# Kernel optimization log

Measured on AMD Instinct MI355X. Metric: run time of the kernel, lower is better.

The kernel has to match this reference:

```python
import jax, jax.numpy as jnp
import numpy as np
import math

L, H, NH, DH, E, FF, A, I = 3, 1024, 8, 128, 768, 4096, 100, 50
B, S = 4, 1024
EPS = 1e-5


def _ln(x, g, b):
    m = jnp.mean(x, -1, keepdims=True)
    v = jnp.var(x, -1, keepdims=True)
    return (x - m) * jax.lax.rsqrt(v + EPS) * g + b


def _pos_encoding(seq, d):
    pos = jnp.arange(seq, dtype=jnp.float32)[:, None]
    div = jnp.exp(jnp.arange(0, d, 2, dtype=jnp.float32) * (-math.log(10000.0) / d))
    ang = pos * div  # [S, d/2]
    return jnp.stack([jnp.sin(ang), jnp.cos(ang)], axis=-1).reshape(seq, d)


def setup_inputs() -> dict:
    key = jax.random.key(0)
    ks = jax.random.split(key, 40)
    w = lambda k, s: jax.random.normal(k, s, jnp.float32) * 0.02
    z = lambda s: jnp.zeros(s, jnp.float32)
    d = {}
    d['frame_embeddings'] = jax.random.normal(ks[0], (B, S, E), jnp.float32)
    d['W_in'] = w(ks[1], (H, E)); d['b_in'] = z((H,))
    # _init_weights sets ALL 'weight' params (incl. LayerNorm) to normal(std=0.02)
    d['ln_in_g'] = w(ks[2], (H,)); d['ln_in_b'] = z((H,))
    d['qkv_w'] = w(ks[3], (L, 3 * H, H)); d['qkv_b'] = z((L, 3 * H))
    d['out_w'] = w(ks[4], (L, H, H)); d['out_b'] = z((L, H))
    d['ff1_w'] = w(ks[5], (L, FF, H)); d['ff1_b'] = z((L, FF))
    d['ff2_w'] = w(ks[6], (L, H, FF)); d['ff2_b'] = z((L, H))
    d['n1_g'] = w(ks[7], (L, H)); d['n1_b'] = z((L, H))
    d['n2_g'] = w(ks[8], (L, H)); d['n2_b'] = z((L, H))
    d['ln_out_g'] = w(ks[9], (H,)); d['ln_out_b'] = z((H,))
    d['a1_w'] = w(ks[10], (H, H)); d['a1_b'] = z((H,))
    d['a2_w'] = w(ks[11], (A, H)); d['a2_b'] = z((A,))
    d['i1_w'] = w(ks[12], (H, H)); d['i1_b'] = z((H,))
    d['i2_w'] = w(ks[13], (I, H)); d['i2_b'] = z((I,))
    d['c1_w'] = w(ks[14], (H // 2, H)); d['c1_b'] = z((H // 2,))
    d['c2_w'] = w(ks[15], (1, H // 2)); d['c2_b'] = z((1,))
    d['p_w'] = w(ks[16], (1, H)); d['p_b'] = z((1,))
    d['smoothing_factor'] = jnp.float32(0.7)
    return d


def _encoder_layer(x, qkv_w, qkv_b, out_w, out_b, ff1_w, ff1_b, ff2_w, ff2_b, n1_g, n1_b, n2_g, n2_b):
    # PyTorch post-norm TransformerEncoderLayer (eval: no dropout)
    b, s, _ = x.shape
    qkv = x @ qkv_w.T + qkv_b  # [B,S,3H]
    q, k, v = jnp.split(qkv, 3, axis=-1)
    q = q.reshape(b, s, NH, DH)
    k = k.reshape(b, s, NH, DH)
    v = v.reshape(b, s, NH, DH)
    scores = jnp.einsum('bqhd,bkhd->bhqk', q, k) / math.sqrt(DH)
    attn = jax.nn.softmax(scores, axis=-1)
    ctx = jnp.einsum('bhqk,bkhd->bqhd', attn, v).reshape(b, s, H)
    x = _ln(x + (ctx @ out_w.T + out_b), n1_g, n1_b)
    ff = jax.nn.gelu(x @ ff1_w.T + ff1_b, approximate=False) @ ff2_w.T + ff2_b
    return _ln(x + ff, n2_g, n2_b)


def reference(frame_embeddings, W_in, b_in, ln_in_g, ln_in_b, qkv_w, qkv_b, out_w, out_b,
              ff1_w, ff1_b, ff2_w, ff2_b, n1_g, n1_b, n2_g, n2_b, ln_out_g, ln_out_b,
              a1_w, a1_b, a2_w, a2_b, i1_w, i1_b, i2_w, i2_b, c1_w, c1_b, c2_w, c2_b,
              p_w, p_b, smoothing_factor):
    b, s, _ = frame_embeddings.shape
    h = frame_embeddings @ W_in.T + b_in
    h = h + _pos_encoding(s, H)[None]
    h = _ln(h, ln_in_g, ln_in_b)
    for l in range(L):
        h = _encoder_layer(h, qkv_w[l], qkv_b[l], out_w[l], out_b[l], ff1_w[l], ff1_b[l],
                           ff2_w[l], ff2_b[l], n1_g[l], n1_b[l], n2_g[l], n2_b[l])
    ctx = _ln(h, ln_out_g, ln_out_b)
    action = jax.nn.gelu(ctx @ a1_w.T + a1_b, approximate=False) @ a2_w.T + a2_b  # [B,S,A]
    instr = jax.nn.gelu(ctx @ i1_w.T + i1_b, approximate=False) @ i2_w.T + i2_b  # [B,S,I]
    conf = jax.nn.sigmoid(jax.nn.gelu(ctx @ c1_w.T + c1_b, approximate=False) @ c2_w.T + c2_b)
    # EMA smoothing over time as a single scan (replaces the per-step Python loop)
    sf = jnp.clip(smoothing_factor, 0.0, 1.0)
    both = jnp.concatenate([action, instr], axis=-1)  # [B,S,A+I]
    def step(carry, xt):
        sm = sf * xt + (1.0 - sf) * carry
        return sm, sm
    _, ys = jax.lax.scan(step, both[:, 0], jnp.swapaxes(both[:, 1:], 0, 1))
    smoothed = jnp.concatenate([both[:, :1], jnp.swapaxes(ys, 0, 1)], axis=1)
    action = smoothed[..., :A]
    instr = smoothed[..., A:]
    pool = jax.nn.softmax(ctx @ p_w.T + p_b, axis=1)  # [B,S,1]
    global_ctx = jnp.einsum('bsi,bsh->bih', pool, ctx)[:, 0]  # [B,H]
    return action, instr, conf, pool[..., 0], global_ctx
```

## Files before the change

kernel.cpp:

```cpp
#include <hip/hip_runtime.h>

typedef __attribute__((ext_vector_type(8))) short frag8;
typedef __attribute__((ext_vector_type(4))) float facc4;

#define MFMA16(a,b,c) __builtin_amdgcn_mfma_f32_16x16x32_bf16((a),(b),(c),0,0,0)

__device__ __forceinline__ unsigned short f2bf(float f){
  unsigned int u = __builtin_bit_cast(unsigned int, f);
  u += 0x7FFFu + ((u >> 16) & 1u);
  return (unsigned short)(u >> 16);
}
__device__ __forceinline__ float bf2f(unsigned short h){
  unsigned int u = ((unsigned int)h) << 16;
  return __builtin_bit_cast(float, u);
}
__device__ __forceinline__ float gelu_f(float x){
  return 0.5f * x * (1.0f + erff(x * 0.70710678118654752440f));
}
__device__ __forceinline__ void gload16(const void* g, void* l){
  __builtin_amdgcn_global_load_lds(
      (const __attribute__((address_space(1))) void*)g,
      (__attribute__((address_space(3))) void*)l, 16, 0, 0);
}

struct CvtSeg { const float* src; unsigned short* dst; long total; long blk_start; int rows_src; int K; };
struct CvtArgs { CvtSeg seg[12]; int nseg; };

__global__ void convert_all(CvtArgs a){
  long blk = blockIdx.x;
  int si = 0;
  for (int i = 1; i < a.nseg; i++) if (blk >= a.seg[i].blk_start) si = i;
  CvtSeg s = a.seg[si];
  long i = ((blk - s.blk_start) * 256 + threadIdx.x) * 4L;
  if (i >= s.total) return;
  long row = i / s.K;
  ushort4 o;
  if (row < s.rows_src){
    float4 v = *(const float4*)(s.src + i);
    o.x = f2bf(v.x); o.y = f2bf(v.y); o.z = f2bf(v.z); o.w = f2bf(v.w);
  } else { o.x = 0; o.y = 0; o.z = 0; o.w = 0; }
  *(ushort4*)(s.dst + i) = o;
}

__global__ void pe_kernel(float* __restrict__ pe){
  const int s = blockIdx.x;
  const int t = threadIdx.x;
  float4 o;
#pragma unroll
  for (int e = 0; e < 4; e++){
    int c = t * 4 + e;
    int i2 = c & ~1;
    float dv = expf(-0.0089944730195080f * (float)i2);
    float ang = (float)s * dv;
    ((float*)&o)[e] = (c & 1) ? cosf(ang) : sinf(ang);
  }
  *(float4*)(pe + (size_t)s * 1024 + t * 4) = o;
}

template<int EPI>
__global__ __launch_bounds__(256, 2)
void gemm_bt(const unsigned short* __restrict__ A,
             const unsigned short* __restrict__ W,
             const float* __restrict__ bias,
             void* __restrict__ Cout,
             int K, int ldC, int coloff, int nvalid)
{
  __shared__ unsigned short As[128 * 32];
  __shared__ unsigned short Bs[128 * 32];
  const int tid = threadIdx.x;
  const int w = tid >> 6, lane = tid & 63;
  const int lh = lane & 15, lq = lane >> 4;
  const int wr = w >> 1, wc = w & 1;
  const long row0 = (long)blockIdx.x * 128;
  const long col0 = (long)blockIdx.y * 128;

  facc4 acc[4][4];
  const facc4 vz = {0.f, 0.f, 0.f, 0.f};
#pragma unroll
  for (int r = 0; r < 4; r++)
#pragma unroll
    for (int c = 0; c < 4; c++) acc[r][c] = vz;

  const int arow = w * 16 + (lane >> 2);
  const int aseg = (lane & 3) * 8;
  const unsigned short* A0 = A + (row0 + arow) * (long)K + aseg;
  const unsigned short* A1 = A + (row0 + 64 + arow) * (long)K + aseg;
  const unsigned short* W0 = W + (col0 + arow) * (long)K + aseg;
  const unsigned short* W1 = W + (col0 + 64 + arow) * (long)K + aseg;
  char* lA0 = (char*)As + w * 1024;
  char* lA1 = (char*)As + 4096 + w * 1024;
  char* lB0 = (char*)Bs + w * 1024;
  char* lB1 = (char*)Bs + 4096 + w * 1024;

  for (int k0 = 0; k0 < K; k0 += 32){
    gload16(A0 + k0, lA0);
    gload16(A1 + k0, lA1);
    gload16(W0 + k0, lB0);
    gload16(W1 + k0, lB1);
    __syncthreads();
    frag8 af[4], bf[4];
#pragma unroll
    for (int r = 0; r < 4; r++) af[r] = *(const frag8*)&As[(wr * 64 + r * 16 + lh) * 32 + lq * 8];
#pragma unroll
    for (int c = 0; c < 4; c++) bf[c] = *(const frag8*)&Bs[(wc * 64 + c * 16 + lh) * 32 + lq * 8];
#pragma unroll
    for (int r = 0; r < 4; r++)
#pragma unroll
      for (int c = 0; c < 4; c++)
        acc[r][c] = MFMA16(af[r], bf[c], acc[r][c]);
    __syncthreads();
  }

#pragma unroll
  for (int c = 0; c < 4; c++){
    const int colt = wc * 64 + c * 16 + lh;
    const long gcol = col0 + colt;
    const bool ok = gcol < nvalid;
    const float bv = ok ? bias[gcol] : 0.f;
#pragma unroll
    for (int r = 0; r < 4; r++){
#pragma unroll
      for (int j = 0; j < 4; j++){
        if (!ok) continue;
        const long grow = row0 + wr * 64 + r * 16 + lq * 4 + j;
        float v = acc[r][c][j] + bv;
        if (EPI == 2) v = gelu_f(v);
        const long off = grow * (long)ldC + coloff + gcol;
        if (EPI == 0) ((float*)Cout)[off] = v;
        else          ((unsigned short*)Cout)[off] = f2bf(v);
      }
    }
  }
}

__global__ __launch_bounds__(256)
void ln_kernel(const float* __restrict__ a, const float* __restrict__ bsrc, int bmode,
               const float* __restrict__ g, const float* __restrict__ be,
               float* __restrict__ of32, unsigned short* __restrict__ obf)
{
  const int row = blockIdx.x;
  const int t = threadIdx.x;
  float4 x = ((const float4*)(a + (size_t)row * 1024))[t];
  if (bmode){
    const size_t brow = (bmode == 1) ? (size_t)row : (size_t)(row & 1023);
    float4 y = ((const float4*)(bsrc + brow * 1024))[t];
    x.x += y.x; x.y += y.y; x.z += y.z; x.w += y.w;
  }
  float s = x.x + x.y + x.z + x.w;
  float ss = x.x * x.x + x.y * x.y + x.z * x.z + x.w * x.w;
#pragma unroll
  for (int mk = 1; mk < 64; mk <<= 1){ s += __shfl_xor(s, mk); ss += __shfl_xor(ss, mk); }
  __shared__ float red[8];
  const int w = t >> 6, lane = t & 63;
  if (lane == 0){ red[w] = s; red[4 + w] = ss; }
  __syncthreads();
  s = red[0] + red[1] + red[2] + red[3];
  ss = red[4] + red[5] + red[6] + red[7];
  const float mean = s * (1.f / 1024.f);
  const float var = ss * (1.f / 1024.f) - mean * mean;
  const float rstd = rsqrtf(var + 1e-5f);
  float4 gg = ((const float4*)g)[t];
  float4 bb = ((const float4*)be)[t];
  float4 o;
  o.x = (x.x - mean) * rstd * gg.x + bb.x;
  o.y = (x.y - mean) * rstd * gg.y + bb.y;
  o.z = (x.z - mean) * rstd * gg.z + bb.z;
  o.w = (x.w - mean) * rstd * gg.w + bb.w;
  if (of32) ((float4*)(of32 + (size_t)row * 1024))[t] = o;
  if (obf){
    ushort4 hh;
    hh.x = f2bf(o.x); hh.y = f2bf(o.y); hh.z = f2bf(o.z); hh.w = f2bf(o.w);
    ((ushort4*)(obf + (size_t)row * 1024))[t] = hh;
  }
}

__global__ void transpose_v(const unsigned short* __restrict__ qkv, unsigned short* __restrict__ vt){
  __shared__ unsigned short t[32][33];
  const int s0 = blockIdx.x * 32;
  const int d0 = blockIdx.y * 32;
  const int bh = blockIdx.z;
  const int b = bh >> 3, h = bh & 7;
  const int tx = threadIdx.x, ty = threadIdx.y;
#pragma unroll
  for (int j = 0; j < 4; j++){
    int srow = ty + j * 8;
    t[srow][tx] = qkv[(size_t)(b * 1024 + s0 + srow) * 3072 + 2048 + h * 128 + d0 + tx];
  }
  __syncthreads();
#pragma unroll
  for (int j = 0; j < 4; j++){
    int drow = ty + j * 8;
    vt[((size_t)bh * 128 + d0 + drow) * 1024 + s0 + tx] = t[tx][drow];
  }
}

__global__ __launch_bounds__(256, 1)
void attn_kernel(const unsigned short* __restrict__ qkv,
                 const unsigned short* __restrict__ vt,
                 unsigned short* __restrict__ ctx)
{
  const int qt = blockIdx.x, h = blockIdx.y, b = blockIdx.z;
  const int tid = threadIdx.x;
  const int w = tid >> 6, lane = tid & 63;
  const int lh = lane & 15, lq = lane >> 4;
  __shared__ unsigned short P[4][32][136];

  const float scale = 0.08838834764831845f;
  const size_t qbase = (size_t)b * 1024 * 3072 + (size_t)h * 128;
  const int q0 = qt * 128 + w * 32;

  frag8 qf[2][4];
#pragma unroll
  for (int r = 0; r < 2; r++)
#pragma unroll
    for (int kk = 0; kk < 4; kk++)
      qf[r][kk] = *(const frag8*)(qkv + qbase + (size_t)(q0 + r * 16 + lh) * 3072 + kk * 32 + lq * 8);

  facc4 O[2][8];
  const facc4 vz = {0.f, 0.f, 0.f, 0.f};
#pragma unroll
  for (int r = 0; r < 2; r++)
#pragma unroll
    for (int c = 0; c < 8; c++) O[r][c] = vz;
  float m[2][4], l[2][4];
#pragma unroll
  for (int r = 0; r < 2; r++)
#pragma unroll
    for (int j = 0; j < 4; j++){ m[r][j] = -3.0e38f; l[r][j] = 0.f; }

  for (int kv0 = 0; kv0 < 1024; kv0 += 128){
    facc4 S[2][8];
#pragma unroll
    for (int r = 0; r < 2; r++)
#pragma unroll
      for (int c = 0; c < 8; c++) S[r][c] = vz;
#pragma unroll
    for (int c = 0; c < 8; c++){
      frag8 kf[4];
#pragma unroll
      for (int kk = 0; kk < 4; kk++)
        kf[kk] = *(const frag8*)(qkv + qbase + 1024 + (size_t)(kv0 + c * 16 + lh) * 3072 + kk * 32 + lq * 8);
#pragma unroll
      for (int kk = 0; kk < 4; kk++)
#pragma unroll
        for (int r = 0; r < 2; r++)
          S[r][c] = MFMA16(qf[r][kk], kf[kk], S[r][c]);
    }
    float tmax[2][4];
#pragma unroll
    for (int r = 0; r < 2; r++)
#pragma unroll
      for (int j = 0; j < 4; j++) tmax[r][j] = -3.0e38f;
#pragma unroll
    for (int r = 0; r < 2; r++)
#pragma unroll
      for (int c = 0; c < 8; c++)
#pragma unroll
        for (int j = 0; j < 4; j++){
          float v = S[r][c][j] * scale;
          S[r][c][j] = v;
          tmax[r][j] = fmaxf(tmax[r][j], v);
        }
#pragma unroll
    for (int mk = 1; mk < 16; mk <<= 1)
#pragma unroll
      for (int r = 0; r < 2; r++)
#pragma unroll
        for (int j = 0; j < 4; j++)
          tmax[r][j] = fmaxf(tmax[r][j], __shfl_xor(tmax[r][j], mk));
    float al[2][4], rs[2][4];
#pragma unroll
    for (int r = 0; r < 2; r++)
#pragma unroll
      for (int j = 0; j < 4; j++){
        float mn = fmaxf(m[r][j], tmax[r][j]);
        al[r][j] = __expf(m[r][j] - mn);
        m[r][j] = mn;
        rs[r][j] = 0.f;
      }
#pragma unroll
    for (int r = 0; r < 2; r++)
#pragma unroll
      for (int c = 0; c < 8; c++)
#pragma unroll
        for (int j = 0; j < 4; j++){
          float p = __expf(S[r][c][j] - m[r][j]);
          S[r][c][j] = p;
          rs[r][j] += p;
        }
#pragma unroll
    for (int mk = 1; mk < 16; mk <<= 1)
#pragma unroll
      for (int r = 0; r < 2; r++)
#pragma unroll
        for (int j = 0; j < 4; j++)
          rs[r][j] += __shfl_xor(rs[r][j], mk);
#pragma unroll
    for (int r = 0; r < 2; r++)
#pragma unroll
      for (int j = 0; j < 4; j++) l[r][j] = l[r][j] * al[r][j] + rs[r][j];
#pragma unroll
    for (int r = 0; r < 2; r++)
#pragma unroll
      for (int c = 0; c < 8; c++)
#pragma unroll
        for (int j = 0; j < 4; j++) O[r][c][j] *= al[r][j];
#pragma unroll
    for (int r = 0; r < 2; r++)
#pragma unroll
      for (int c = 0; c < 8; c++)
#pragma unroll
        for (int j = 0; j < 4; j++)
          P[w][r * 16 + lq * 4 + j][c * 16 + lh] = f2bf(S[r][c][j]);
    frag8 pf[2][4];
#pragma unroll
    for (int r = 0; r < 2; r++)
#pragma unroll
      for (int kk = 0; kk < 4; kk++)
        pf[r][kk] = *(const frag8*)&P[w][r * 16 + lh][kk * 32 + lq * 8];
#pragma unroll
    for (int c2 = 0; c2 < 8; c2++){
      frag8 vf[4];
#pragma unroll
      for (int kk = 0; kk < 4; kk++)
        vf[kk] = *(const frag8*)(vt + ((size_t)(b * 8 + h) * 128 + c2 * 16 + lh) * 1024 + kv0 + kk * 32 + lq * 8);
#pragma unroll
      for (int kk = 0; kk < 4; kk++)
#pragma unroll
        for (int r = 0; r < 2; r++)
          O[r][c2] = MFMA16(pf[r][kk], vf[kk], O[r][c2]);
    }
  }
#pragma unroll
  for (int r = 0; r < 2; r++)
#pragma unroll
    for (int c2 = 0; c2 < 8; c2++)
#pragma unroll
      for (int j = 0; j < 4; j++)
        P[w][r * 16 + lq * 4 + j][c2 * 16 + lh] = f2bf(O[r][c2][j] / l[r][j]);
  for (int rr = 0; rr < 32; rr++){
    const int token = b * 1024 + qt * 128 + w * 32 + rr;
    const unsigned int val = *(const unsigned int*)&P[w][rr][lane * 2];
    *(unsigned int*)(ctx + (size_t)token * 1024 + h * 128 + lane * 2) = val;
  }
}

__global__ void ema_kernel(const float* __restrict__ both, const float* __restrict__ sfp,
                           float* __restrict__ oact, float* __restrict__ oinst)
{
  const int idx = blockIdx.x * 256 + threadIdx.x;
  if (idx >= 4 * 1024 * 150) return;
  const int c = idx % 150;
  const int bs = idx / 150;
  const int s = bs & 1023;
  float sf = fminf(fmaxf(sfp[0], 0.f), 1.f);
  const float q = 1.f - sf;
  const float* p = both + (size_t)bs * 160 + c;
  float acc = 0.f, wgt = sf;
  const int klim = (s < 28) ? s : 28;
  for (int k = 0; k < klim; k++){ acc += wgt * p[-(long)k * 160]; wgt *= q; }
  if (s <= 28) acc += powf(q, (float)s) * p[-(long)s * 160];
  if (c < 100) oact[(size_t)bs * 100 + c] = acc;
  else         oinst[(size_t)bs * 50 + (c - 100)] = acc;
}

__global__ void head_c2(const unsigned short* __restrict__ x, const float* __restrict__ wv,
                        const float* __restrict__ bv, float* __restrict__ out)
{
  const int row = blockIdx.x * 4 + (threadIdx.x >> 6);
  const int lane = threadIdx.x & 63;
  float acc = 0.f;
#pragma unroll
  for (int i = 0; i < 8; i++){
    int cidx = i * 64 + lane;
    acc += bf2f(x[(size_t)row * 512 + cidx]) * wv[cidx];
  }
#pragma unroll
  for (int mk = 1; mk < 64; mk <<= 1) acc += __shfl_xor(acc, mk);
  if (lane == 0) out[row] = 1.f / (1.f + __expf(-(acc + bv[0])));
}

__global__ void head_p(const float* __restrict__ x, const float* __restrict__ wv,
                       const float* __restrict__ bv, float* __restrict__ out)
{
  const int row = blockIdx.x * 4 + (threadIdx.x >> 6);
  const int lane = threadIdx.x & 63;
  float acc = 0.f;
#pragma unroll
  for (int i = 0; i < 16; i++){
    int cidx = i * 64 + lane;
    acc += x[(size_t)row * 1024 + cidx] * wv[cidx];
  }
#pragma unroll
  for (int mk = 1; mk < 64; mk <<= 1) acc += __shfl_xor(acc, mk);
  if (lane == 0) out[row] = acc + bv[0];
}

__global__ void pool_softmax(const float* __restrict__ scores, float* __restrict__ poolws,
                             float* __restrict__ outpool)
{
  const int b = blockIdx.x, t = threadIdx.x;
  float4 v = ((const float4*)(scores + (size_t)b * 1024))[t];
  float mx = fmaxf(fmaxf(v.x, v.y), fmaxf(v.z, v.w));
#pragma unroll
  for (int mk = 1; mk < 64; mk <<= 1) mx = fmaxf(mx, __shfl_xor(mx, mk));
  __shared__ float red[8];
  const int w = t >> 6, lane = t & 63;
  if (lane == 0) red[w] = mx;
  __syncthreads();
  mx = fmaxf(fmaxf(red[0], red[1]), fmaxf(red[2], red[3]));
  float4 e;
  e.x = __expf(v.x - mx); e.y = __expf(v.y - mx); e.z = __expf(v.z - mx); e.w = __expf(v.w - mx);
  float sum = e.x + e.y + e.z + e.w;
#pragma unroll
  for (int mk = 1; mk < 64; mk <<= 1) sum += __shfl_xor(sum, mk);
  if (lane == 0) red[4 + w] = sum;
  __syncthreads();
  sum = red[4] + red[5] + red[6] + red[7];
  const float inv = 1.f / sum;
  e.x *= inv; e.y *= inv; e.z *= inv; e.w *= inv;
  ((float4*)(poolws + (size_t)b * 1024))[t] = e;
  ((float4*)(outpool + (size_t)b * 1024))[t] = e;
}

__global__ void globalctx_kernel(const float* __restrict__ pool, const float* __restrict__ ctxf,
                                 float* __restrict__ out)
{
  const int hh = blockIdx.x * 256 + threadIdx.x;
  const int b = blockIdx.y;
  const float* p = pool + (size_t)b * 1024;
  const float* c = ctxf + (size_t)b * 1024 * 1024 + hh;
  float acc = 0.f;
  for (int s = 0; s < 1024; s++) acc += p[s] * c[(size_t)s * 1024];
  out[(size_t)b * 1024 + hh] = acc;
}

extern "C" void kernel_launch(void* const* d_in, const int* in_sizes, int n_in,
                              void* d_out, int out_size, void* d_ws, size_t ws_size,
                              hipStream_t stream)
{
  if (n_in < 34) return;
  const float* emb     = (const float*)d_in[0];
  const float* W_in    = (const float*)d_in[1];
  const float* b_in    = (const float*)d_in[2];
  const float* ln_in_g = (const float*)d_in[3];
  const float* ln_in_b = (const float*)d_in[4];
  const float* qkv_w   = (const float*)d_in[5];
  const float* qkv_b   = (const float*)d_in[6];
  const float* out_w   = (const float*)d_in[7];
  const float* out_b   = (const float*)d_in[8];
  const float* ff1_w   = (const float*)d_in[9];
  const float* ff1_b   = (const float*)d_in[10];
  const float* ff2_w   = (const float*)d_in[11];
  const float* ff2_b   = (const float*)d_in[12];
  const float* n1_g    = (const float*)d_in[13];
  const float* n1_b    = (const float*)d_in[14];
  const float* n2_g    = (const float*)d_in[15];
  const float* n2_b    = (const float*)d_in[16];
  const float* ln_out_g= (const float*)d_in[17];
  const float* ln_out_b= (const float*)d_in[18];
  const float* a1_w    = (const float*)d_in[19];
  const float* a1_b    = (const float*)d_in[20];
  const float* a2_w    = (const float*)d_in[21];
  const float* a2_b    = (const float*)d_in[22];
  const float* i1_w    = (const float*)d_in[23];
  const float* i1_b    = (const float*)d_in[24];
  const float* i2_w    = (const float*)d_in[25];
  const float* i2_b    = (const float*)d_in[26];
  const float* c1_w    = (const float*)d_in[27];
  const float* c1_b    = (const float*)d_in[28];
  const float* c2_w    = (const float*)d_in[29];
  const float* c2_b    = (const float*)d_in[30];
  const float* p_w     = (const float*)d_in[31];
  const float* p_b     = (const float*)d_in[32];
  const float* sfp     = (const float*)d_in[33];

  char* ws = (char*)d_ws;
  size_t off = 0;
  auto alloc = [&](size_t bytes) -> void* {
    void* p = ws + off;
    off += (bytes + 255) & ~(size_t)255;
    return p;
  };
  unsigned short* emb_bf  = (unsigned short*)alloc((size_t)4096 * 768 * 2);
  unsigned short* Win_bf  = (unsigned short*)alloc((size_t)1024 * 768 * 2);
  unsigned short* qkvw_bf = (unsigned short*)alloc((size_t)3 * 3072 * 1024 * 2);
  unsigned short* outw_bf = (unsigned short*)alloc((size_t)3 * 1024 * 1024 * 2);
  unsigned short* ff1w_bf = (unsigned short*)alloc((size_t)3 * 4096 * 1024 * 2);
  unsigned short* ff2w_bf = (unsigned short*)alloc((size_t)3 * 1024 * 4096 * 2);
  unsigned short* a1w_bf  = (unsigned short*)alloc((size_t)1024 * 1024 * 2);
  unsigned short* a2w_bf  = (unsigned short*)alloc((size_t)128 * 1024 * 2);
  unsigned short* i1w_bf  = (unsigned short*)alloc((size_t)1024 * 1024 * 2);
  unsigned short* i2w_bf  = (unsigned short*)alloc((size_t)128 * 1024 * 2);
  unsigned short* c1w_bf  = (unsigned short*)alloc((size_t)512 * 1024 * 2);
  float* pe      = (float*)alloc((size_t)1024 * 1024 * 4);
  float* t0      = (float*)alloc((size_t)4096 * 1024 * 4);
  float* hres    = (float*)alloc((size_t)4096 * 1024 * 4);
  unsigned short* h_bf = (unsigned short*)alloc((size_t)4096 * 1024 * 2);
  unsigned short* buf1 = (unsigned short*)alloc((size_t)4096 * 4096 * 2);
  unsigned short* vtb  = (unsigned short*)alloc((size_t)4096 * 1024 * 2);
  unsigned short* ctxb = (unsigned short*)alloc((size_t)4096 * 1024 * 2);
  float* bothb  = (float*)alloc((size_t)4096 * 160 * 4);
  float* scores = (float*)alloc((size_t)4096 * 4);
  float* poolws = (float*)alloc((size_t)4096 * 4);
  if (off > ws_size) return;

  float* out_action = (float*)d_out;
  float* out_instr  = out_action + 4 * 1024 * 100;
  float* out_conf   = out_instr + 4 * 1024 * 50;
  float* out_pool   = out_conf + 4 * 1024;
  float* out_gctx   = out_pool + 4 * 1024;

  CvtArgs ca{};
  long blk = 0;
  auto addseg = [&](const float* src, unsigned short* dst, long rows_src, long rows_dst, long Kd){
    CvtSeg& sg = ca.seg[ca.nseg];
    sg.src = src; sg.dst = dst; sg.total = rows_dst * Kd;
    sg.rows_src = (int)rows_src; sg.K = (int)Kd; sg.blk_start = blk;
    blk += (sg.total + 1023) / 1024;
    ca.nseg++;
  };
  addseg(emb,   emb_bf,  4096, 4096, 768);
  addseg(W_in,  Win_bf,  1024, 1024, 768);
  addseg(qkv_w, qkvw_bf, 9216, 9216, 1024);
  addseg(out_w, outw_bf, 3072, 3072, 1024);
  addseg(ff1_w, ff1w_bf, 12288, 12288, 1024);
  addseg(ff2_w, ff2w_bf, 3072, 3072, 4096);
  addseg(a1_w,  a1w_bf,  1024, 1024, 1024);
  addseg(a2_w,  a2w_bf,  100,  128,  1024);
  addseg(i1_w,  i1w_bf,  1024, 1024, 1024);
  addseg(i2_w,  i2w_bf,  50,   128,  1024);
  addseg(c1_w,  c1w_bf,  512,  512,  1024);
  convert_all<<<dim3((unsigned)blk), dim3(256), 0, stream>>>(ca);

  pe_kernel<<<dim3(1024), dim3(256), 0, stream>>>(pe);

  gemm_bt<0><<<dim3(32, 8), dim3(256), 0, stream>>>(emb_bf, Win_bf, b_in, t0, 768, 1024, 0, 1024);
  ln_kernel<<<dim3(4096), dim3(256), 0, stream>>>(t0, pe, 2, ln_in_g, ln_in_b, hres, h_bf);

  for (int l = 0; l < 3; l++){
    gemm_bt<1><<<dim3(32, 24), dim3(256), 0, stream>>>(h_bf, qkvw_bf + (size_t)l * 3072 * 1024,
                                                       qkv_b + (size_t)l * 3072, buf1, 1024, 3072, 0, 3072);
    transpose_v<<<dim3(32, 4, 32), dim3(32, 8), 0, stream>>>(buf1, vtb);
    attn_kernel<<<dim3(8, 8, 4), dim3(256), 0, stream>>>(buf1, vtb, ctxb);
    gemm_bt<0><<<dim3(32, 8), dim3(256), 0, stream>>>(ctxb, outw_bf + (size_t)l * 1024 * 1024,
                                                      out_b + (size_t)l * 1024, t0, 1024, 1024, 0, 1024);
    ln_kernel<<<dim3(4096), dim3(256), 0, stream>>>(hres, t0, 1, n1_g + l * 1024, n1_b + l * 1024, hres, h_bf);
    gemm_bt<2><<<dim3(32, 32), dim3(256), 0, stream>>>(h_bf, ff1w_bf + (size_t)l * 4096 * 1024,
                                                       ff1_b + (size_t)l * 4096, buf1, 1024, 4096, 0, 4096);
    gemm_bt<0><<<dim3(32, 8), dim3(256), 0, stream>>>(buf1, ff2w_bf + (size_t)l * 1024 * 4096,
                                                      ff2_b + (size_t)l * 1024, t0, 4096, 1024, 0, 1024);
    ln_kernel<<<dim3(4096), dim3(256), 0, stream>>>(hres, t0, 1, n2_g + l * 1024, n2_b + l * 1024, hres, h_bf);
  }

  ln_kernel<<<dim3(4096), dim3(256), 0, stream>>>(hres, nullptr, 0, ln_out_g, ln_out_b, t0, ctxb);

  gemm_bt<2><<<dim3(32, 8), dim3(256), 0, stream>>>(ctxb, a1w_bf, a1_b, vtb, 1024, 1024, 0, 1024);
  gemm_bt<0><<<dim3(32, 1), dim3(256), 0, stream>>>(vtb, a2w_bf, a2_b, bothb, 1024, 160, 0, 100);
  gemm_bt<2><<<dim3(32, 8), dim3(256), 0, stream>>>(ctxb, i1w_bf, i1_b, vtb, 1024, 1024, 0, 1024);
  gemm_bt<0><<<dim3(32, 1), dim3(256), 0, stream>>>(vtb, i2w_bf, i2_b, bothb, 1024, 160, 100, 50);
  gemm_bt<2><<<dim3(32, 4), dim3(256), 0, stream>>>(ctxb, c1w_bf, c1_b, vtb, 1024, 512, 0, 512);
  head_c2<<<dim3(1024), dim3(256), 0, stream>>>(vtb, c2_w, c2_b, out_conf);
  head_p<<<dim3(1024), dim3(256), 0, stream>>>(t0, p_w, p_b, scores);
  pool_softmax<<<dim3(4), dim3(256), 0, stream>>>(scores, poolws, out_pool);
  globalctx_kernel<<<dim3(4, 4), dim3(256), 0, stream>>>(poolws, t0, out_gctx);
  ema_kernel<<<dim3(2400), dim3(256), 0, stream>>>(bothb, sfp, out_action, out_instr);
}
```

Baseline: 1.164 ms.

## Stage K/V tiles in swizzled LDS with double-buffered async loads in attention

The attention kernel now loads 64-row K and V tiles cooperatively into XOR-swizzled LDS buffers using global_load_lds, double-buffered so the next tile's load overlaps compute on the current one. Before, each wave read K and V straight from global memory. Each wave now handles 16 query rows instead of 32, and the grid doubles to 512 blocks with launch bounds raised to allow two blocks per CU, for better occupancy and latency hiding. The cost is halved Q reuse per K/V load, a barrier every iteration, and more LDS per block.

New measurement: 1.069 ms. 8.1% less time.

```diff
diff --git a/kernel.cpp b/kernel.cpp
--- a/kernel.cpp
+++ b/kernel.cpp
@@ -194,7 +194,7 @@
   }
 }
 
-__global__ __launch_bounds__(256, 1)
+__global__ __launch_bounds__(256, 2)
 void attn_kernel(const unsigned short* __restrict__ qkv,
                  const unsigned short* __restrict__ vt,
                  unsigned short* __restrict__ ctx)
@@ -203,145 +203,145 @@
   const int tid = threadIdx.x;
   const int w = tid >> 6, lane = tid & 63;
   const int lh = lane & 15, lq = lane >> 4;
-  __shared__ unsigned short P[4][32][136];
+
+  __shared__ unsigned short Ks[2][64 * 128];
+  __shared__ unsigned short Vs[2][128 * 64];
+  __shared__ unsigned short P[4][16][72];
 
   const float scale = 0.08838834764831845f;
-  const size_t qbase = (size_t)b * 1024 * 3072 + (size_t)h * 128;
-  const int q0 = qt * 128 + w * 32;
-
-  frag8 qf[2][4];
-#pragma unroll
-  for (int r = 0; r < 2; r++)
-#pragma unroll
-    for (int kk = 0; kk < 4; kk++)
-      qf[r][kk] = *(const frag8*)(qkv + qbase + (size_t)(q0 + r * 16 + lh) * 3072 + kk * 32 + lq * 8);
-
-  facc4 O[2][8];
+  const int q0 = qt * 64 + w * 16;
+
+  frag8 qf[4];
+#pragma unroll
+  for (int kk = 0; kk < 4; kk++)
+    qf[kk] = *(const frag8*)(qkv + ((size_t)(b * 1024 + q0 + lh)) * 3072 + h * 128 + kk * 32 + lq * 8);
+
+  const unsigned short* Kg = qkv + (size_t)b * 1024 * 3072 + 1024 + h * 128;
+  const unsigned short* Vg = vt + (size_t)(b * 8 + h) * 128 * 1024;
+
+  const int k_rsub = lane >> 4;
+  const int k_c    = lane & 15;
+  const int v_rsub = lane >> 3;
+  const int v_c    = lane & 7;
+
+  auto stage = [&](int buf, int kv0){
+#pragma unroll
+    for (int i = 0; i < 4; i++){
+      const int seg = i * 4 + w;
+      const int kr = seg * 4 + k_rsub;
+      const int ksc = k_c ^ (kr & 7);
+      gload16(Kg + (size_t)(kv0 + kr) * 3072 + ksc * 8,
+              (char*)Ks + buf * 16384 + seg * 1024);
+      const int vr = seg * 8 + v_rsub;
+      const int vsc = v_c ^ (vr & 7);
+      gload16(Vg + (size_t)vr * 1024 + kv0 + vsc * 8,
+              (char*)Vs + buf * 16384 + seg * 1024);
+    }
+  };
+
+  facc4 O[8];
   const facc4 vz = {0.f, 0.f, 0.f, 0.f};
 #pragma unroll
-  for (int r = 0; r < 2; r++)
-#pragma unroll
-    for (int c = 0; c < 8; c++) O[r][c] = vz;
-  float m[2][4], l[2][4];
-#pragma unroll
-  for (int r = 0; r < 2; r++)
-#pragma unroll
-    for (int j = 0; j < 4; j++){ m[r][j] = -3.0e38f; l[r][j] = 0.f; }
-
-  for (int kv0 = 0; kv0 < 1024; kv0 += 128){
-    facc4 S[2][8];
-#pragma unroll
-    for (int r = 0; r < 2; r++)
-#pragma unroll
-      for (int c = 0; c < 8; c++) S[r][c] = vz;
-#pragma unroll
-    for (int c = 0; c < 8; c++){
-      frag8 kf[4];
-#pragma unroll
-      for (int kk = 0; kk < 4; kk++)
-        kf[kk] = *(const frag8*)(qkv + qbase + 1024 + (size_t)(kv0 + c * 16 + lh) * 3072 + kk * 32 + lq * 8);
-#pragma unroll
-      for (int kk = 0; kk < 4; kk++)
-#pragma unroll
-        for (int r = 0; r < 2; r++)
-          S[r][c] = MFMA16(qf[r][kk], kf[kk], S[r][c]);
+  for (int c = 0; c < 8; c++) O[c] = vz;
+  float m[4], l[4];
+#pragma unroll
+  for (int j = 0; j < 4; j++){ m[j] = -3.0e38f; l[j] = 0.f; }
+
+  stage(0, 0);
+  __syncthreads();
+
+  for (int t = 0; t < 16; t++){
+    const int cur = t & 1;
+    if (t < 15) stage(cur ^ 1, (t + 1) * 64);
+
+    facc4 S[4];
+#pragma unroll
+    for (int c = 0; c < 4; c++) S[c] = vz;
+    const char* Kb = (const char*)Ks + cur * 16384;
+#pragma unroll
+    for (int c = 0; c < 4; c++){
+      const int row = c * 16 + lh;
+#pragma unroll
+      for (int kk = 0; kk < 4; kk++){
+        frag8 kf = *(const frag8*)(Kb + row * 256 + ((kk * 64 + lq * 16) ^ ((row & 7) << 4)));
+        S[c] = MFMA16(qf[kk], kf, S[c]);
+      }
     }
-    float tmax[2][4];
-#pragma unroll
-    for (int r = 0; r < 2; r++)
-#pragma unroll
-      for (int j = 0; j < 4; j++) tmax[r][j] = -3.0e38f;
-#pragma unroll
-    for (int r = 0; r < 2; r++)
-#pragma unroll
-      for (int c = 0; c < 8; c++)
-#pragma unroll
-        for (int j = 0; j < 4; j++){
-          float v = S[r][c][j] * scale;
-          S[r][c][j] = v;
-          tmax[r][j] = fmaxf(tmax[r][j], v);
-        }
+    float tmax[4] = {-3.0e38f, -3.0e38f, -3.0e38f, -3.0e38f};
+#pragma unroll
+    for (int c = 0; c < 4; c++)
+#pragma unroll
+      for (int j = 0; j < 4; j++){
+        float v = S[c][j] * scale;
+        S[c][j] = v;
+        tmax[j] = fmaxf(tmax[j], v);
+      }
 #pragma unroll
     for (int mk = 1; mk < 16; mk <<= 1)
 #pragma unroll
-      for (int r = 0; r < 2; r++)
-#pragma unroll
-        for (int j = 0; j < 4; j++)
-          tmax[r][j] = fmaxf(tmax[r][j], __shfl_xor(tmax[r][j], mk));
-    float al[2][4], rs[2][4];
-#pragma unroll
-    for (int r = 0; r < 2; r++)
+      for (int j = 0; j < 4; j++) tmax[j] = fmaxf(tmax[j], __shfl_xor(tmax[j], mk));
+    float al[4], rs[4];
+#pragma unroll
+    for (int j = 0; j < 4; j++){
+      float mn = fmaxf(m[j], tmax[j]);
+      al[j] = __expf(m[j] - mn);
+      m[j] = mn;
+      rs[j] = 0.f;
+    }
+#pragma unroll
+    for (int c = 0; c < 4; c++)
 #pragma unroll
       for (int j = 0; j < 4; j++){
-        float mn = fmaxf(m[r][j], tmax[r][j]);
-        al[r][j] = __expf(m[r][j] - mn);
-        m[r][j] = mn;
-        rs[r][j] = 0.f;
+        float p = __expf(S[c][j] - m[j]);
+        S[c][j] = p;
+        rs[j] += p;
       }
 #pragma unroll
-    for (int r = 0; r < 2; r++)
-#pragma unroll
-      for (int c = 0; c < 8; c++)
-#pragma unroll
-        for (int j = 0; j < 4; j++){
-          float p = __expf(S[r][c][j] - m[r][j]);
-          S[r][c][j] = p;
-          rs[r][j] += p;
-        }
-#pragma unroll
     for (int mk = 1; mk < 16; mk <<= 1)
 #pragma unroll
-      for (int r = 0; r < 2; r++)
-#pragma unroll
-        for (int j = 0; j < 4; j++)
-          rs[r][j] += __shfl_xor(rs[r][j], mk);
-#pragma unroll
-    for (int r = 0; r < 2; r++)
-#pragma unroll
-      for (int j = 0; j < 4; j++) l[r][j] = l[r][j] * al[r][j] + rs[r][j];
-#pragma unroll
-    for (int r = 0; r < 2; r++)
-#pragma unroll
-      for (int c = 0; c < 8; c++)
-#pragma unroll
-        for (int j = 0; j < 4; j++) O[r][c][j] *= al[r][j];
-#pragma unroll
-    for (int r = 0; r < 2; r++)
-#pragma unroll
-      for (int c = 0; c < 8; c++)
-#pragma unroll
-        for (int j = 0; j < 4; j++)
-          P[w][r * 16 + lq * 4 + j][c * 16 + lh] = f2bf(S[r][c][j]);
-    frag8 pf[2][4];
-#pragma unroll
-    for (int r = 0; r < 2; r++)
-#pragma unroll
-      for (int kk = 0; kk < 4; kk++)
-        pf[r][kk] = *(const frag8*)&P[w][r * 16 + lh][kk * 32 + lq * 8];
+      for (int j = 0; j < 4; j++) rs[j] += __shfl_xor(rs[j], mk);
+#pragma unroll
+    for (int j = 0; j < 4; j++) l[j] = l[j] * al[j] + rs[j];
+#pragma unroll
+    for (int c = 0; c < 8; c++)
+#pragma unroll
+      for (int j = 0; j < 4; j++) O[c][j] *= al[j];
+
+#pragma unroll
+    for (int c = 0; c < 4; c++)
+#pragma unroll
+      for (int j = 0; j < 4; j++)
+        P[w][lq * 4 + j][c * 16 + lh] = f2bf(S[c][j]);
+    frag8 pf[2];
+#pragma unroll
+    for (int kk = 0; kk < 2; kk++)
+      pf[kk] = *(const frag8*)&P[w][lh][kk * 32 + lq * 8];
+
+    const char* Vb = (const char*)Vs + cur * 16384;
 #pragma unroll
     for (int c2 = 0; c2 < 8; c2++){
-      frag8 vf[4];
-#pragma unroll
-      for (int kk = 0; kk < 4; kk++)
-        vf[kk] = *(const frag8*)(vt + ((size_t)(b * 8 + h) * 128 + c2 * 16 + lh) * 1024 + kv0 + kk * 32 + lq * 8);
-#pragma unroll
-      for (int kk = 0; kk < 4; kk++)
-#pragma unroll
-        for (int r = 0; r < 2; r++)
-          O[r][c2] = MFMA16(pf[r][kk], vf[kk], O[r][c2]);
+      const int row = c2 * 16 + lh;
+#pragma unroll
+      for (int kk = 0; kk < 2; kk++){
+        frag8 vf = *(const frag8*)(Vb + row * 128 + ((kk * 64 + lq * 16) ^ ((row & 7) << 4)));
+        O[c2] = MFMA16(pf[kk], vf, O[c2]);
+      }
     }
-  }
-#pragma unroll
-  for (int r = 0; r < 2; r++)
-#pragma unroll
-    for (int c2 = 0; c2 < 8; c2++)
-#pragma unroll
-      for (int j = 0; j < 4; j++)
-        P[w][r * 16 + lq * 4 + j][c2 * 16 + lh] = f2bf(O[r][c2][j] / l[r][j]);
-  for (int rr = 0; rr < 32; rr++){
-    const int token = b * 1024 + qt * 128 + w * 32 + rr;
-    const unsigned int val = *(const unsigned int*)&P[w][rr][lane * 2];
-    *(unsigned int*)(ctx + (size_t)token * 1024 + h * 128 + lane * 2) = val;
+    __syncthreads();
+  }
+
+  unsigned short* Es = (unsigned short*)Ks;
+#pragma unroll
+  for (int c2 = 0; c2 < 8; c2++)
+#pragma unroll
+    for (int j = 0; j < 4; j++)
+      Es[w * 2048 + (lq * 4 + j) * 128 + c2 * 16 + lh] = f2bf(O[c2][j] / l[j]);
+  __syncthreads();
+  const int token0 = b * 1024 + qt * 64 + w * 16;
+#pragma unroll
+  for (int rr = 0; rr < 16; rr++){
+    const unsigned int val = *(const unsigned int*)&Es[w * 2048 + rr * 128 + lane * 2];
+    *(unsigned int*)(ctx + (size_t)(token0 + rr) * 1024 + h * 128 + lane * 2) = val;
   }
 }
 
@@ -542,7 +542,7 @@
     gemm_bt<1><<<dim3(32, 24), dim3(256), 0, stream>>>(h_bf, qkvw_bf + (size_t)l * 3072 * 1024,
                                                        qkv_b + (size_t)l * 3072, buf1, 1024, 3072, 0, 3072);
     transpose_v<<<dim3(32, 4, 32), dim3(32, 8), 0, stream>>>(buf1, vtb);
-    attn_kernel<<<dim3(8, 8, 4), dim3(256), 0, stream>>>(buf1, vtb, ctxb);
+    attn_kernel<<<dim3(16, 8, 4), dim3(256), 0, stream>>>(buf1, vtb, ctxb);
     gemm_bt<0><<<dim3(32, 8), dim3(256), 0, stream>>>(ctxb, outw_bf + (size_t)l * 1024 * 1024,
                                                       out_b + (size_t)l * 1024, t0, 1024, 1024, 0, 1024);
     ln_kernel<<<dim3(4096), dim3(256), 0, stream>>>(hres, t0, 1, n1_g + l * 1024, n1_b + l * 1024, hres, h_bf);
```
